# Performance work log

Hardware: AMD Instinct MI355X
Metric: run time of the kernel (lower is better)

Reference implementation:

```python
import jax, jax.numpy as jnp
import numpy as np
from jax import lax

EPS = 1e-12  # F.normalize eps


def conv3x3(x, w, b):
    # x [B,C,H,W], w [O,C,3,3], b [O]
    y = lax.conv_general_dilated(x, w, window_strides=(1, 1), padding=((1, 1), (1, 1)),
                                 dimension_numbers=("NCHW", "OIHW", "NCHW"))
    return y + b[None, :, None, None]


def bilinear_sample(img, py, px):
    # img [B,C,H,W]; py,px [B,H,W] fractional pixel coords; zero outside.
    B, C, H, W = img.shape
    y0 = jnp.floor(py)
    x0 = jnp.floor(px)
    img_flat = img.reshape(B, C, H * W)
    out = jnp.zeros_like(img)
    for dy in (0, 1):
        for dx in (0, 1):
            yi = y0 + dy
            xi = x0 + dx
            wgt = (1.0 - jnp.abs(py - yi)) * (1.0 - jnp.abs(px - xi))
            valid = (yi >= 0) & (yi < H) & (xi >= 0) & (xi < W)
            yc = jnp.clip(yi, 0, H - 1).astype(jnp.int32)
            xc = jnp.clip(xi, 0, W - 1).astype(jnp.int32)
            idx = (yc * W + xc).reshape(B, 1, H * W)
            v = jnp.take_along_axis(img_flat, idx, axis=2).reshape(B, C, H, W)
            out = out + v * (wgt * valid.astype(img.dtype))[:, None]
    return out


def deform_conv3x3(x, offset, weight):
    # torchvision deform_conv2d, k=3, stride=1, pad=1, no mask (modulator unused in source).
    # offset [B, 18, H, W]: per kernel tap k -> (dy=offset[:,2k], dx=offset[:,2k+1])
    B, Cin, H, W = x.shape
    iy = jnp.arange(H, dtype=x.dtype)[:, None]
    ix = jnp.arange(W, dtype=x.dtype)[None, :]
    out = jnp.zeros((B, weight.shape[0], H, W), dtype=x.dtype)
    for k in range(9):
        kh, kw = k // 3, k % 3
        py = iy - 1 + kh + offset[:, 2 * k]
        px = ix - 1 + kw + offset[:, 2 * k + 1]
        s = bilinear_sample(x, py, px)  # [B,Cin,H,W]
        out = out + jnp.einsum("bchw,oc->bohw", s, weight[:, :, kh, kw])
    return out


def l2norm_lastdim(t):
    n = jnp.sqrt(jnp.sum(t * t, axis=-1, keepdims=True))
    return t / jnp.maximum(n, EPS)


def setup_inputs() -> dict:
    key = jax.random.key(0)
    ks = jax.random.split(key, 8)
    B, C, H, W = 2, 192, 128, 128
    heads = 4
    s = 0.02
    return {
        "x": jax.random.normal(ks[0], (B, C, H, W), jnp.float32),
        "q": jax.random.normal(ks[1], (B, C, H, W), jnp.float32),
        "temperature": jnp.ones((1, heads, 1, 1), jnp.float32),
        "kv_w": jax.random.normal(ks[2], (2 * C, C), jnp.float32) * s,
        "offset_w": jax.random.normal(ks[3], (18, 2 * C, 3, 3), jnp.float32) * 0.001,
        "offset_b": jax.random.normal(ks[4], (18,), jnp.float32) * 0.1,
        "reg_w": jax.random.normal(ks[5], (2 * C, 2 * C, 3, 3), jnp.float32) * s,
        "proj_w": jax.random.normal(ks[6], (C, C), jnp.float32) * s,
    }


def reference(x, q, temperature, kv_w, offset_w, offset_b, reg_w, proj_w):
    B, C, H, W = x.shape
    heads = temperature.shape[1]
    n = H * W
    # kv 1x1 conv
    kv = jnp.einsum("bchw,oc->bohw", x, kv_w)  # [B,2C,H,W]
    # deformable conv KV path
    offset = conv3x3(kv, offset_w, offset_b)  # [B,18,H,W]
    kv = deform_conv3x3(kv, offset, reg_w)  # [B,2C,H,W]
    k, v = jnp.split(kv, 2, axis=1)
    qh = q.reshape(B, heads, C // heads, n)
    kh = k.reshape(B, heads, C // heads, n)
    vh = v.reshape(B, heads, C // heads, n)
    qh = l2norm_lastdim(qh)
    kh = l2norm_lastdim(kh)
    attn = jax.nn.softmax(jnp.einsum("bhdn,bhen->bhde", qh, kh) * temperature, axis=-1)
    out = jnp.einsum("bhde,bhen->bhdn", attn, vh).reshape(B, C, H, W)
    out = jnp.einsum("bchw,oc->bohw", out, proj_w)
    return (out, qh)
```

## Files before the change

kernel.cpp:

```cpp
#include <hip/hip_runtime.h>
#include <math.h>

#define B_ 2
#define C_ 192
#define C2_ 384
#define H_ 128
#define W_ 128
#define N_ (H_*W_)
#define HEADS_ 4
#define HD_ 48
#define EPS_ 1e-12f

typedef __bf16 bf16x8 __attribute__((ext_vector_type(8)));
typedef float  f32x4  __attribute__((ext_vector_type(4)));

__global__ __launch_bounds__(256) void k_pack(const float* __restrict__ regw, const float* __restrict__ kvw,
                                              const float* __restrict__ offw,
                                              ushort* __restrict__ regwP, ushort* __restrict__ kvwP,
                                              ushort* __restrict__ offwP) {
    const int NR = 9 * 12 * C2_ * 32;
    const int NK = 6 * C2_ * 32;
    const int NO = 12 * 9 * 32 * 32;
    int idx = blockIdx.x * 256 + threadIdx.x;
    union { __bf16 h; ushort u; } cv;
    if (idx < NR) {
        int t  = idx / (12 * C2_ * 32);
        int r  = idx - t * (12 * C2_ * 32);
        int ci = r / (C2_ * 32);
        int r2 = r - ci * (C2_ * 32);
        int oc = r2 >> 5;
        int kk = r2 & 31;
        cv.h = (__bf16)regw[(oc * C2_ + ci * 32 + kk) * 9 + t];
        regwP[idx] = cv.u;
    } else if (idx < NR + NK) {
        int r  = idx - NR;
        int ci = r / (C2_ * 32);
        int r2 = r - ci * (C2_ * 32);
        int oc = r2 >> 5;
        int kk = r2 & 31;
        cv.h = (__bf16)kvw[oc * C_ + ci * 32 + kk];
        kvwP[r] = cv.u;
    } else if (idx < NR + NK + NO) {
        int r  = idx - NR - NK;
        int ci = r / (9 * 32 * 32);
        int r2 = r - ci * (9 * 32 * 32);
        int t  = r2 / (32 * 32);
        int r3 = r2 - t * (32 * 32);
        int oc = r3 >> 5;
        int kk = r3 & 31;
        float v = (oc < 18) ? offw[(oc * C2_ + ci * 32 + kk) * 9 + t] : 0.f;
        cv.h = (__bf16)v;
        offwP[r] = cv.u;
    }
}

__global__ __launch_bounds__(256) void k_kv1x1_mfma(const float* __restrict__ x, const __bf16* __restrict__ kvwP,
                                                    __bf16* __restrict__ kvB) {
    __shared__ __bf16 As[64 * 40];
    __shared__ __bf16 Ws[C2_ * 40];
    const int bid = blockIdx.x;
    const int swz = (bid & 7) * 64 + (bid >> 3);
    const int b   = swz >> 8;
    const int p0  = (swz & 255) * 64;
    const int tid  = threadIdx.x;
    const int wv   = tid >> 6;
    const int lane = tid & 63;
    const int fr   = lane & 15;
    const int fg   = lane >> 4;
    const int apx  = tid & 63;
    const int akg  = tid >> 6;

    f32x4 acc[4][6];
    #pragma unroll
    for (int mg = 0; mg < 4; ++mg)
        #pragma unroll
        for (int ng = 0; ng < 6; ++ng) acc[mg][ng] = (f32x4){0.f, 0.f, 0.f, 0.f};

    for (int ci = 0; ci < 6; ++ci) {
        const int cc = ci * 32;
        const __bf16* wsrc = kvwP + (size_t)ci * C2_ * 32;
        #pragma unroll
        for (int i = 0; i < 6; ++i) {
            const int e = tid + i * 256;
            const int oc = e >> 2, sg = e & 3;
            *(bf16x8*)&Ws[oc * 40 + sg * 8] = *(const bf16x8*)(wsrc + oc * 32 + sg * 8);
        }
        {
            float v[8];
            #pragma unroll
            for (int j = 0; j < 8; ++j)
                v[j] = x[((size_t)b * C_ + cc + akg * 8 + j) * N_ + p0 + apx];
            bf16x8 pk = {(__bf16)v[0], (__bf16)v[1], (__bf16)v[2], (__bf16)v[3],
                         (__bf16)v[4], (__bf16)v[5], (__bf16)v[6], (__bf16)v[7]};
            *(bf16x8*)&As[apx * 40 + akg * 8] = pk;
        }
        __syncthreads();
        bf16x8 a[4];
        #pragma unroll
        for (int mg = 0; mg < 4; ++mg)
            a[mg] = *(const bf16x8*)&As[(mg * 16 + fr) * 40 + fg * 8];
        #pragma unroll
        for (int ng = 0; ng < 6; ++ng) {
            const bf16x8 bb = *(const bf16x8*)&Ws[(wv * 96 + ng * 16 + fr) * 40 + fg * 8];
            #pragma unroll
            for (int mg = 0; mg < 4; ++mg)
                acc[mg][ng] = __builtin_amdgcn_mfma_f32_16x16x32_bf16(a[mg], bb, acc[mg][ng], 0, 0, 0);
        }
        __syncthreads();
    }
    #pragma unroll
    for (int mg = 0; mg < 4; ++mg)
        #pragma unroll
        for (int j = 0; j < 4; ++j) {
            const int p = p0 + mg * 16 + fg * 4 + j;
            __bf16* dst = kvB + ((size_t)b * N_ + p) * C2_ + wv * 96 + fr;
            #pragma unroll
            for (int ng = 0; ng < 6; ++ng)
                dst[ng * 16] = (__bf16)acc[mg][ng][j];
        }
}

__global__ __launch_bounds__(256) void k_qnorm(const float* __restrict__ q, float* __restrict__ qn,
                                               __bf16* __restrict__ qnB) {
    const int row = blockIdx.x;
    const float* src = q + (size_t)row * N_;
    float* dst = qn + (size_t)row * N_;
    __bf16* dstB = qnB + (size_t)row * N_;
    float ss = 0.f;
    for (int i = threadIdx.x; i < N_ / 4; i += 256) {
        float4 v = ((const float4*)src)[i];
        ss += v.x * v.x + v.y * v.y + v.z * v.z + v.w * v.w;
    }
    __shared__ float red[256];
    red[threadIdx.x] = ss;
    __syncthreads();
    for (int s = 128; s > 0; s >>= 1) {
        if (threadIdx.x < s) red[threadIdx.x] += red[threadIdx.x + s];
        __syncthreads();
    }
    float rn = 1.f / fmaxf(sqrtf(red[0]), EPS_);
    for (int i = threadIdx.x; i < N_ / 8; i += 256) {
        float4 v0 = ((const float4*)src)[2 * i];
        float4 v1 = ((const float4*)src)[2 * i + 1];
        float f0 = v0.x * rn, f1 = v0.y * rn, f2 = v0.z * rn, f3 = v0.w * rn;
        float f4 = v1.x * rn, f5 = v1.y * rn, f6 = v1.z * rn, f7 = v1.w * rn;
        ((float4*)dst)[2 * i]     = make_float4(f0, f1, f2, f3);
        ((float4*)dst)[2 * i + 1] = make_float4(f4, f5, f6, f7);
        bf16x8 pk = {(__bf16)f0, (__bf16)f1, (__bf16)f2, (__bf16)f3,
                     (__bf16)f4, (__bf16)f5, (__bf16)f6, (__bf16)f7};
        *(bf16x8*)&dstB[i * 8] = pk;
    }
}

__global__ __launch_bounds__(256) void k_offconv_mfma(const __bf16* __restrict__ kvB, const __bf16* __restrict__ offwP,
                                                      const float* __restrict__ offb, float* __restrict__ offT) {
    __shared__ __bf16 Win[3 * 66 * 40];
    __shared__ __bf16 Wall[9 * 32 * 40];
    const int bid = blockIdx.x;
    const int swz = (bid & 7) * 64 + (bid >> 3);
    const int b   = swz >> 8;
    const int p0  = (swz & 255) * 64;
    const int y   = p0 >> 7;
    const int x0  = p0 & 127;
    const int tid  = threadIdx.x;
    const int wv   = tid >> 6;
    const int lane = tid & 63;
    const int fr   = lane & 15;
    const int fg   = lane >> 4;
    const __bf16* kb = kvB + (size_t)b * N_ * C2_;

    f32x4 acc[2];
    acc[0] = (f32x4){0.f, 0.f, 0.f, 0.f};
    acc[1] = (f32x4){0.f, 0.f, 0.f, 0.f};

    for (int ci = 0; ci < 12; ++ci) {
        const int cc = ci * 32;
        for (int e = tid; e < 3 * 66 * 4; e += 256) {
            const int r  = e / 264;
            const int rem = e - r * 264;
            const int cw = rem >> 2;
            const int sg = rem & 3;
            const int gy = y - 1 + r;
            const int gx = x0 - 1 + cw;
            bf16x8 v = {};
            if ((unsigned)gy < H_ && (unsigned)gx < W_)
                v = *(const bf16x8*)(kb + ((size_t)(gy * W_ + gx)) * C2_ + cc + sg * 8);
            *(bf16x8*)&Win[(r * 66 + cw) * 40 + sg * 8] = v;
        }
        const __bf16* wsrc = offwP + (size_t)ci * 9 * 32 * 32;
        for (int e = tid; e < 9 * 32 * 4; e += 256) {
            const int t  = e >> 7;
            const int r2 = e & 127;
            const int oc = r2 >> 2;
            const int sg = r2 & 3;
            *(bf16x8*)&Wall[(t * 32 + oc) * 40 + sg * 8] = *(const bf16x8*)(wsrc + (t * 32 + oc) * 32 + sg * 8);
        }
        __syncthreads();
        #pragma unroll
        for (int t = 0; t < 9; ++t) {
            const int dy = t / 3, dx = t % 3;
            const bf16x8 a = *(const bf16x8*)&Win[((dy * 66) + (wv * 16 + fr + dx)) * 40 + fg * 8];
            #pragma unroll
            for (int ng = 0; ng < 2; ++ng) {
                const bf16x8 bb = *(const bf16x8*)&Wall[(t * 32 + ng * 16 + fr) * 40 + fg * 8];
                acc[ng] = __builtin_amdgcn_mfma_f32_16x16x32_bf16(a, bb, acc[ng], 0, 0, 0);
            }
        }
        __syncthreads();
    }
    #pragma unroll
    for (int ng = 0; ng < 2; ++ng) {
        const int oc = ng * 16 + fr;
        if (oc < 18) {
            const float bias = offb[oc];
            #pragma unroll
            for (int j = 0; j < 4; ++j) {
                const int p = p0 + wv * 16 + fg * 4 + j;
                offT[((size_t)b * N_ + p) * 18 + oc] = acc[ng][j] + bias;
            }
        }
    }
}

#define SAMPLE_A(ITN, NB) do {                                                           \
    const int tt_ = (ITN) / 12, ci_ = (ITN) - tt_ * 12;                                  \
    const __bf16* cb_ = kb + ci_ * 32 + ssub;                                            \
    float s_[8] = {0.f,0.f,0.f,0.f,0.f,0.f,0.f,0.f};                                     \
    _Pragma("unroll")                                                                    \
    for (int j_ = 0; j_ < 4; ++j_) {                                                     \
        const float w_ = sh.m.wwt[tt_][spx][j_];                                         \
        const bf16x8 v_ = *(const bf16x8*)(cb_ + (size_t)sh.m.widx[tt_][spx][j_] * C2_); \
        _Pragma("unroll")                                                                \
        for (int e_ = 0; e_ < 8; ++e_) s_[e_] += w_ * (float)v_[e_];                     \
    }                                                                                    \
    bf16x8 pk_ = {(__bf16)s_[0],(__bf16)s_[1],(__bf16)s_[2],(__bf16)s_[3],               \
                  (__bf16)s_[4],(__bf16)s_[5],(__bf16)s_[6],(__bf16)s_[7]};              \
    *(bf16x8*)&sh.m.As[NB][spx * 40 + ssub] = pk_;                                       \
} while (0)

#define DEF_BODY(CUR, NXT) do {                                                          \
    const int itn_ = (it < 107) ? it + 1 : 107;                                          \
    {   const __bf16* wb_ = wbase + (size_t)itn_ * (C2_ * 32);                           \
        _Pragma("unroll")                                                                \
        for (int ng_ = 0; ng_ < 6; ++ng_)                                                \
            bfr[NXT][ng_] = *(const bf16x8*)(wb_ + ng_ * 512); }                         \
    bf16x8 a_[4];                                                                        \
    _Pragma("unroll")                                                                    \
    for (int mg_ = 0; mg_ < 4; ++mg_)                                                    \
        a_[mg_] = *(const bf16x8*)&sh.m.As[CUR][(mg_ * 16 + fr) * 40 + fg * 8];          \
    SAMPLE_A(itn_, NXT);                                                                 \
    _Pragma("unroll")                                                                    \
    for (int ng_ = 0; ng_ < 6; ++ng_)                                                    \
        _Pragma("unroll")                                                                \
        for (int mg_ = 0; mg_ < 4; ++mg_)                                                \
            acc[mg_][ng_] = __builtin_amdgcn_mfma_f32_16x16x32_bf16(a_[mg_], bfr[CUR][ng_], acc[mg_][ng_], 0, 0, 0); \
    __syncthreads();                                                                     \
    ++it;                                                                                \
} while (0)

__global__ __launch_bounds__(256, 2) void k_deform_mfma(const __bf16* __restrict__ kvB, const float* __restrict__ offT,
                                                        const __bf16* __restrict__ regwP,
                                                        __bf16* __restrict__ kT, __bf16* __restrict__ vP) {
    __shared__ union {
        struct {
            __bf16 As[2][64 * 40];
            float  wwt[9][64][4];
            int    widx[9][64][4];
        } m;
        __bf16 kTs[192 * 72];
    } sh;
    const int bid = blockIdx.x;
    const int swz = (bid & 7) * 64 + (bid >> 3);
    const int b   = swz >> 8;
    const int p0  = (swz & 255) * 64;
    const int tid  = threadIdx.x;
    const int wv   = tid >> 6;
    const int lane = tid & 63;
    const int fr   = lane & 15;
    const int fg   = lane >> 4;
    const int spx  = tid >> 2;
    const int ssub = (tid & 3) * 8;
    const __bf16* kb    = kvB + (size_t)b * N_ * C2_;
    const __bf16* wbase = regwP + ((size_t)(wv * 96 + fr)) * 32 + fg * 8;

    f32x4 acc[4][6];
    #pragma unroll
    for (int mg = 0; mg < 4; ++mg)
        #pragma unroll
        for (int ng = 0; ng < 6; ++ng) acc[mg][ng] = (f32x4){0.f, 0.f, 0.f, 0.f};

    for (int e = tid; e < 576; e += 256) {
        const int tt = e >> 6, pp = e & 63;
        const int p = p0 + pp;
        const int yy = p >> 7, xx = p & 127;
        const float dy = offT[((size_t)b * N_ + p) * 18 + 2 * tt];
        const float dx = offT[((size_t)b * N_ + p) * 18 + 2 * tt + 1];
        const float py = (float)(yy + tt / 3 - 1) + dy;
        const float px = (float)(xx + tt % 3 - 1) + dx;
        const float fy = floorf(py), fx = floorf(px);
        const int y0 = (int)fy, x0i = (int)fx;
        const float ay = py - fy, ax = px - fx;
        #pragma unroll
        for (int j = 0; j < 4; ++j) {
            const int yi = y0 + (j >> 1);
            const int xi = x0i + (j & 1);
            const float wj = ((j >> 1) ? ay : 1.f - ay) * ((j & 1) ? ax : 1.f - ax);
            const bool v = ((unsigned)yi < H_) && ((unsigned)xi < W_);
            sh.m.wwt[tt][pp][j]  = v ? wj : 0.f;
            sh.m.widx[tt][pp][j] = v ? (yi * W_ + xi) : 0;
        }
    }
    bf16x8 bfr[2][6];
    #pragma unroll
    for (int ng = 0; ng < 6; ++ng) bfr[0][ng] = *(const bf16x8*)(wbase + ng * 512);
    __syncthreads();
    SAMPLE_A(0, 0);
    __syncthreads();

    int it = 0;
    for (int i2 = 0; i2 < 54; ++i2) {
        DEF_BODY(0, 1);
        DEF_BODY(1, 0);
    }

    __syncthreads();
    if (wv < 2) {
        #pragma unroll
        for (int mg = 0; mg < 4; ++mg)
            #pragma unroll
            for (int ng = 0; ng < 6; ++ng) {
                const int oc = wv * 96 + ng * 16 + fr;
                #pragma unroll
                for (int j = 0; j < 4; ++j)
                    sh.kTs[oc * 72 + mg * 16 + fg * 4 + j] = (__bf16)acc[mg][ng][j];
            }
    } else {
        #pragma unroll
        for (int mg = 0; mg < 4; ++mg)
            #pragma unroll
            for (int j = 0; j < 4; ++j) {
                const int p = p0 + mg * 16 + fg * 4 + j;
                __bf16* dst = vP + ((size_t)b * N_ + p) * C_ + (wv - 2) * 96 + fr;
                #pragma unroll
                for (int ng = 0; ng < 6; ++ng)
                    dst[ng * 16] = (__bf16)acc[mg][ng][j];
            }
    }
    __syncthreads();
    for (int e = tid; e < 192 * 8; e += 256) {
        const int oc = e >> 3, sub = e & 7;
        *(bf16x8*)&kT[((size_t)b * C_ + oc) * N_ + p0 + sub * 8] = *(const bf16x8*)&sh.kTs[oc * 72 + sub * 8];
    }
}

__global__ __launch_bounds__(256) void k_knorm2(const __bf16* __restrict__ kT, float* __restrict__ knorm) {
    const int row = blockIdx.x;
    const __bf16* src = kT + (size_t)row * N_;
    float ss = 0.f;
    for (int i = threadIdx.x; i < N_ / 8; i += 256) {
        const bf16x8 v = ((const bf16x8*)src)[i];
        #pragma unroll
        for (int e = 0; e < 8; ++e) { float f = (float)v[e]; ss += f * f; }
    }
    __shared__ float red[256];
    red[threadIdx.x] = ss;
    __syncthreads();
    for (int s = 128; s > 0; s >>= 1) {
        if (threadIdx.x < s) red[threadIdx.x] += red[threadIdx.x + s];
        __syncthreads();
    }
    if (threadIdx.x == 0) knorm[row] = 1.f / fmaxf(sqrtf(red[0]), EPS_);
}

__global__ __launch_bounds__(256) void k_attn_mfma(const __bf16* __restrict__ qnB, const __bf16* __restrict__ kT,
                                                   float* __restrict__ part) {
    const int bh = blockIdx.y;
    const int b  = bh >> 2, h = bh & 3;
    const int wv = threadIdx.x >> 6, lane = threadIdx.x & 63;
    const int sl = blockIdx.x * 4 + wv;
    const int n0 = sl * 128;
    const int fr = lane & 15, fg = lane >> 4;
    const __bf16* qb = qnB + ((size_t)b * C_ + h * HD_) * N_ + n0 + fg * 8;
    const __bf16* kb = kT  + ((size_t)b * C_ + h * HD_) * N_ + n0 + fg * 8;
    f32x4 acc[3][3];
    #pragma unroll
    for (int i = 0; i < 3; ++i)
        #pragma unroll
        for (int j = 0; j < 3; ++j) acc[i][j] = (f32x4){0.f, 0.f, 0.f, 0.f};
    #pragma unroll
    for (int kc = 0; kc < 4; ++kc) {
        bf16x8 a[3], bb[3];
        #pragma unroll
        for (int mg = 0; mg < 3; ++mg) a[mg]  = *(const bf16x8*)(qb + (size_t)(mg * 16 + fr) * N_ + kc * 32);
        #pragma unroll
        for (int ng = 0; ng < 3; ++ng) bb[ng] = *(const bf16x8*)(kb + (size_t)(ng * 16 + fr) * N_ + kc * 32);
        #pragma unroll
        for (int mg = 0; mg < 3; ++mg)
            #pragma unroll
            for (int ng = 0; ng < 3; ++ng)
                acc[mg][ng] = __builtin_amdgcn_mfma_f32_16x16x32_bf16(a[mg], bb[ng], acc[mg][ng], 0, 0, 0);
    }
    float* pp = part + ((size_t)bh * 128 + sl) * (HD_ * HD_);
    #pragma unroll
    for (int mg = 0; mg < 3; ++mg)
        #pragma unroll
        for (int ng = 0; ng < 3; ++ng)
            #pragma unroll
            for (int j = 0; j < 4; ++j)
                pp[(mg * 16 + fg * 4 + j) * HD_ + ng * 16 + fr] = acc[mg][ng][j];
}

__global__ __launch_bounds__(256) void k_softmax(const float* __restrict__ part, const float* __restrict__ knorm,
                                                 const float* __restrict__ temp, float* __restrict__ attn) {
    const int row = blockIdx.x;
    const int b = row / (HEADS_ * HD_);
    const int r = row % (HEADS_ * HD_);
    const int h = r / HD_;
    const int d = r % HD_;
    const int bh = b * HEADS_ + h;
    const int wv = threadIdx.x >> 6;
    const int lane = threadIdx.x & 63;
    __shared__ float red[4][HD_];
    if (lane < HD_) {
        const float* pp = part + (size_t)bh * 128 * (HD_ * HD_) + d * HD_ + lane;
        float s = 0.f;
        for (int sl = wv; sl < 128; sl += 4)
            s += pp[(size_t)sl * (HD_ * HD_)];
        red[wv][lane] = s;
    }
    __syncthreads();
    if (wv == 0) {
        float v = -INFINITY;
        if (lane < HD_) {
            float t = red[0][lane] + red[1][lane] + red[2][lane] + red[3][lane];
            v = t * knorm[b * C_ + h * HD_ + lane] * temp[h];
        }
        float m = v;
        #pragma unroll
        for (int off = 32; off > 0; off >>= 1) m = fmaxf(m, __shfl_xor(m, off));
        float ex = (lane < HD_) ? expf(v - m) : 0.f;
        float sum = ex;
        #pragma unroll
        for (int off = 32; off > 0; off >>= 1) sum += __shfl_xor(sum, off);
        if (lane < HD_)
            attn[((size_t)bh * HD_ + d) * HD_ + lane] = ex / sum;
    }
}

__global__ __launch_bounds__(256) void k_m(const float* __restrict__ projw, const float* __restrict__ attn,
                                           __bf16* __restrict__ MmB) {
    const int gid = blockIdx.x * 256 + threadIdx.x;
    if (gid >= B_ * C_ * C_) return;
    const int b  = gid / (C_ * C_);
    const int r  = gid % (C_ * C_);
    const int oc = r / C_;
    const int he = r % C_;
    const int h = he / HD_;
    const int e = he % HD_;
    float s = 0.f;
    #pragma unroll 8
    for (int d = 0; d < HD_; ++d)
        s += projw[oc * C_ + h * HD_ + d] * attn[(((size_t)b * HEADS_ + h) * HD_ + d) * HD_ + e];
    MmB[gid] = (__bf16)s;
}

__global__ __launch_bounds__(256) void k_out_mfma(const __bf16* __restrict__ MmB, const __bf16* __restrict__ vP,
                                                  float* __restrict__ out) {
    const int bid = blockIdx.x;
    const int swz = (bid & 7) * 64 + (bid >> 3);
    const int b   = swz >> 8;
    const int p0  = (swz & 255) * 64;
    const int wv = threadIdx.x >> 6, lane = threadIdx.x & 63;
    const int fr = lane & 15, fg = lane >> 4;
    const __bf16* vb = vP + ((size_t)b * N_ + p0 + wv * 16 + fr) * C_ + fg * 8;
    const __bf16* mb = MmB + ((size_t)b * C_ + fr) * C_ + fg * 8;
    f32x4 acc[12];
    #pragma unroll
    for (int rr = 0; rr < 12; ++rr) acc[rr] = (f32x4){0.f, 0.f, 0.f, 0.f};
    #pragma unroll
    for (int kc = 0; kc < 6; ++kc) {
        const bf16x8 bb = *(const bf16x8*)(vb + kc * 32);
        #pragma unroll
        for (int rr = 0; rr < 12; ++rr) {
            const bf16x8 a = *(const bf16x8*)(mb + (size_t)(rr * 16) * C_ + kc * 32);
            acc[rr] = __builtin_amdgcn_mfma_f32_16x16x32_bf16(a, bb, acc[rr], 0, 0, 0);
        }
    }
    #pragma unroll
    for (int rr = 0; rr < 12; ++rr)
        #pragma unroll
        for (int j = 0; j < 4; ++j)
            out[((size_t)b * C_ + rr * 16 + fg * 4 + j) * N_ + p0 + wv * 16 + fr] = acc[rr][j];
}

extern "C" void kernel_launch(void* const* d_in, const int* in_sizes, int n_in,
                              void* d_out, int out_size, void* d_ws, size_t ws_size,
                              hipStream_t stream) {
    (void)in_sizes; (void)n_in; (void)out_size; (void)ws_size;
    const float* x     = (const float*)d_in[0];
    const float* q     = (const float*)d_in[1];
    const float* temp  = (const float*)d_in[2];
    const float* kvw   = (const float*)d_in[3];
    const float* offw  = (const float*)d_in[4];
    const float* offb  = (const float*)d_in[5];
    const float* regw  = (const float*)d_in[6];
    const float* projw = (const float*)d_in[7];

    float* out = (float*)d_out;
    float* qn  = out + (size_t)B_ * C_ * N_;
    __bf16* kvB = (__bf16*)out;

    ushort* kT    = (ushort*)d_ws;
    ushort* vP    = kT + (size_t)B_ * C_ * N_;
    float*  offT  = (float*)(vP + (size_t)B_ * C_ * N_);
    ushort* regwP = (ushort*)(offT + (size_t)B_ * N_ * 18);
    ushort* kvwP  = regwP + (size_t)9 * 12 * C2_ * 32;
    ushort* offwP = kvwP + (size_t)6 * C2_ * 32;
    ushort* qnB   = offwP + (size_t)12 * 9 * 32 * 32;
    float*  part  = (float*)(qnB + (size_t)B_ * C_ * N_);
    float*  attn  = part + (size_t)B_ * HEADS_ * 128 * HD_ * HD_;
    float*  knorm = attn + (size_t)B_ * HEADS_ * HD_ * HD_;
    ushort* MmB   = (ushort*)(knorm + (size_t)B_ * C_);

    const int packN = 9 * 12 * C2_ * 32 + 6 * C2_ * 32 + 12 * 9 * 32 * 32;
    k_pack<<<dim3((packN + 255) / 256), 256, 0, stream>>>(regw, kvw, offw, regwP, kvwP, offwP);
    k_kv1x1_mfma<<<dim3(N_ / 64 * B_), 256, 0, stream>>>(x, (const __bf16*)kvwP, kvB);
    k_offconv_mfma<<<dim3(N_ / 64 * B_), 256, 0, stream>>>(kvB, (const __bf16*)offwP, offb, offT);
    k_deform_mfma<<<dim3(N_ / 64 * B_), 256, 0, stream>>>(kvB, offT, (const __bf16*)regwP,
                                                          (__bf16*)kT, (__bf16*)vP);
    k_qnorm<<<dim3(B_ * C_), 256, 0, stream>>>(q, qn, (__bf16*)qnB);
    k_knorm2<<<dim3(B_ * C_), 256, 0, stream>>>((const __bf16*)kT, knorm);
    k_attn_mfma<<<dim3(32, B_ * HEADS_), 256, 0, stream>>>((const __bf16*)qnB, (const __bf16*)kT, part);
    k_softmax<<<dim3(B_ * HEADS_ * HD_), 256, 0, stream>>>(part, knorm, temp, attn);
    k_m<<<dim3((B_ * C_ * C_ + 255) / 256), 256, 0, stream>>>(projw, attn, (__bf16*)MmB);
    k_out_mfma<<<dim3(N_ / 64 * B_), 256, 0, stream>>>((const __bf16*)MmB, (const __bf16*)vP, out);
}
```

Measured before the change: 264.8 us.

## Prefetch deformable gather one iteration ahead and vectorize shared-memory loads

The bilinear gather for the deformable-conv A tile is split into an issue step and a pack step, so the global gathers for iteration i+2 are in flight while the MFMAs for iteration i run. Gather indices and weights are now read from shared memory as int4/float4 vectors. The k-transpose store to shared memory is packed into bf16x4 writes. Gather latency is meant to be hidden behind compute, at the cost of holding four more bf16x8 registers in each thread, which could hurt occupancy at launch bounds (256,2).

```diff
diff --git a/kernel.cpp b/kernel.cpp
--- a/kernel.cpp
+++ b/kernel.cpp
@@ -12,6 +12,7 @@
 #define EPS_ 1e-12f
 
 typedef __bf16 bf16x8 __attribute__((ext_vector_type(8)));
+typedef __bf16 bf16x4 __attribute__((ext_vector_type(4)));
 typedef float  f32x4  __attribute__((ext_vector_type(4)));
 
 __global__ __launch_bounds__(256) void k_pack(const float* __restrict__ regw, const float* __restrict__ kvw,
@@ -222,16 +223,26 @@
     }
 }
 
-#define SAMPLE_A(ITN, NB) do {                                                           \
+
+#define ISSUE_GATHER(ITN) do {                                                           \
     const int tt_ = (ITN) / 12, ci_ = (ITN) - tt_ * 12;                                  \
+    const int4 id4_ = *(const int4*)&sh.m.widx[tt_][spx][0];                             \
     const __bf16* cb_ = kb + ci_ * 32 + ssub;                                            \
+    graw[0] = *(const bf16x8*)(cb_ + (size_t)id4_.x * C2_);                              \
+    graw[1] = *(const bf16x8*)(cb_ + (size_t)id4_.y * C2_);                              \
+    graw[2] = *(const bf16x8*)(cb_ + (size_t)id4_.z * C2_);                              \
+    graw[3] = *(const bf16x8*)(cb_ + (size_t)id4_.w * C2_);                              \
+} while (0)
+
+#define PACK_A(ITN, NB) do {                                                             \
+    const int tt_ = (ITN) / 12;                                                          \
+    const float4 w4_ = *(const float4*)&sh.m.wwt[tt_][spx][0];                           \
+    const float wj_[4] = {w4_.x, w4_.y, w4_.z, w4_.w};                                   \
     float s_[8] = {0.f,0.f,0.f,0.f,0.f,0.f,0.f,0.f};                                     \
     _Pragma("unroll")                                                                    \
     for (int j_ = 0; j_ < 4; ++j_) {                                                     \
-        const float w_ = sh.m.wwt[tt_][spx][j_];                                         \
-        const bf16x8 v_ = *(const bf16x8*)(cb_ + (size_t)sh.m.widx[tt_][spx][j_] * C2_); \
         _Pragma("unroll")                                                                \
-        for (int e_ = 0; e_ < 8; ++e_) s_[e_] += w_ * (float)v_[e_];                     \
+        for (int e_ = 0; e_ < 8; ++e_) s_[e_] += wj_[j_] * (float)graw[j_][e_];          \
     }                                                                                    \
     bf16x8 pk_ = {(__bf16)s_[0],(__bf16)s_[1],(__bf16)s_[2],(__bf16)s_[3],               \
                   (__bf16)s_[4],(__bf16)s_[5],(__bf16)s_[6],(__bf16)s_[7]};              \
@@ -239,8 +250,9 @@
 } while (0)
 
 #define DEF_BODY(CUR, NXT) do {                                                          \
-    const int itn_ = (it < 107) ? it + 1 : 107;                                          \
-    {   const __bf16* wb_ = wbase + (size_t)itn_ * (C2_ * 32);                           \
+    const int ip1_ = (it < 107) ? it + 1 : 107;                                          \
+    const int ip2_ = (it < 106) ? it + 2 : 107;                                          \
+    {   const __bf16* wb_ = wbase + (size_t)ip1_ * (C2_ * 32);                           \
         _Pragma("unroll")                                                                \
         for (int ng_ = 0; ng_ < 6; ++ng_)                                                \
             bfr[NXT][ng_] = *(const bf16x8*)(wb_ + ng_ * 512); }                         \
@@ -248,7 +260,8 @@
     _Pragma("unroll")                                                                    \
     for (int mg_ = 0; mg_ < 4; ++mg_)                                                    \
         a_[mg_] = *(const bf16x8*)&sh.m.As[CUR][(mg_ * 16 + fr) * 40 + fg * 8];          \
-    SAMPLE_A(itn_, NXT);                                                                 \
+    PACK_A(ip1_, NXT);                                                                   \
+    ISSUE_GATHER(ip2_);                                                                  \
     _Pragma("unroll")                                                                    \
     for (int ng_ = 0; ng_ < 6; ++ng_)                                                    \
         _Pragma("unroll")                                                                \
@@ -310,11 +323,15 @@
             sh.m.widx[tt][pp][j] = v ? (yi * W_ + xi) : 0;
         }
     }
+    __syncthreads();
+
+    bf16x8 graw[4];
     bf16x8 bfr[2][6];
+    ISSUE_GATHER(0);
+    PACK_A(0, 0);
+    ISSUE_GATHER(1);
     #pragma unroll
     for (int ng = 0; ng < 6; ++ng) bfr[0][ng] = *(const bf16x8*)(wbase + ng * 512);
-    __syncthreads();
-    SAMPLE_A(0, 0);
     __syncthreads();
 
     int it = 0;
@@ -330,9 +347,9 @@
             #pragma unroll
             for (int ng = 0; ng < 6; ++ng) {
                 const int oc = wv * 96 + ng * 16 + fr;
-                #pragma unroll
-                for (int j = 0; j < 4; ++j)
-                    sh.kTs[oc * 72 + mg * 16 + fg * 4 + j] = (__bf16)acc[mg][ng][j];
+                const bf16x4 pk = {(__bf16)acc[mg][ng][0], (__bf16)acc[mg][ng][1],
+                                   (__bf16)acc[mg][ng][2], (__bf16)acc[mg][ng][3]};
+                *(bf16x4*)&sh.kTs[oc * 72 + mg * 16 + fg * 4] = pk;
             }
     } else {
         #pragma unroll
```

New measurement: 250.2 us. -5.5%, faster.

## Restructure deform conv so each wave samples its own pixels and fuse k-norm partials

Applied to the files above, without the earlier changes.

The deformable conv kernel is reorganized so that each wave owns 16 pixels and all 384 output channels. It samples its A fragment straight into registers, removing the shared-memory A double buffer and the per-iteration block barriers. The B weights are now loaded per wave for all 24 N-groups rather than split across waves, which raises global/L2 weight traffic and register pressure. The k-channel sum of squares is computed in the epilogue as per-block partials, so the full pass over kT in the norm kernel becomes a small reduction.

```diff
diff --git a/kernel.cpp b/kernel.cpp
--- a/kernel.cpp
+++ b/kernel.cpp
@@ -12,6 +12,7 @@
 #define EPS_ 1e-12f
 
 typedef __bf16 bf16x8 __attribute__((ext_vector_type(8)));
+typedef __bf16 bf16x4 __attribute__((ext_vector_type(4)));
 typedef float  f32x4  __attribute__((ext_vector_type(4)));
 
 __global__ __launch_bounds__(256) void k_pack(const float* __restrict__ regw, const float* __restrict__ kvw,
@@ -222,72 +223,34 @@
     }
 }
 
-#define SAMPLE_A(ITN, NB) do {                                                           \
-    const int tt_ = (ITN) / 12, ci_ = (ITN) - tt_ * 12;                                  \
-    const __bf16* cb_ = kb + ci_ * 32 + ssub;                                            \
-    float s_[8] = {0.f,0.f,0.f,0.f,0.f,0.f,0.f,0.f};                                     \
-    _Pragma("unroll")                                                                    \
-    for (int j_ = 0; j_ < 4; ++j_) {                                                     \
-        const float w_ = sh.m.wwt[tt_][spx][j_];                                         \
-        const bf16x8 v_ = *(const bf16x8*)(cb_ + (size_t)sh.m.widx[tt_][spx][j_] * C2_); \
-        _Pragma("unroll")                                                                \
-        for (int e_ = 0; e_ < 8; ++e_) s_[e_] += w_ * (float)v_[e_];                     \
-    }                                                                                    \
-    bf16x8 pk_ = {(__bf16)s_[0],(__bf16)s_[1],(__bf16)s_[2],(__bf16)s_[3],               \
-                  (__bf16)s_[4],(__bf16)s_[5],(__bf16)s_[6],(__bf16)s_[7]};              \
-    *(bf16x8*)&sh.m.As[NB][spx * 40 + ssub] = pk_;                                       \
-} while (0)
-
-#define DEF_BODY(CUR, NXT) do {                                                          \
-    const int itn_ = (it < 107) ? it + 1 : 107;                                          \
-    {   const __bf16* wb_ = wbase + (size_t)itn_ * (C2_ * 32);                           \
-        _Pragma("unroll")                                                                \
-        for (int ng_ = 0; ng_ < 6; ++ng_)                                                \
-            bfr[NXT][ng_] = *(const bf16x8*)(wb_ + ng_ * 512); }                         \
-    bf16x8 a_[4];                                                                        \
-    _Pragma("unroll")                                                                    \
-    for (int mg_ = 0; mg_ < 4; ++mg_)                                                    \
-        a_[mg_] = *(const bf16x8*)&sh.m.As[CUR][(mg_ * 16 + fr) * 40 + fg * 8];          \
-    SAMPLE_A(itn_, NXT);                                                                 \
-    _Pragma("unroll")                                                                    \
-    for (int ng_ = 0; ng_ < 6; ++ng_)                                                    \
-        _Pragma("unroll")                                                                \
-        for (int mg_ = 0; mg_ < 4; ++mg_)                                                \
-            acc[mg_][ng_] = __builtin_amdgcn_mfma_f32_16x16x32_bf16(a_[mg_], bfr[CUR][ng_], acc[mg_][ng_], 0, 0, 0); \
-    __syncthreads();                                                                     \
-    ++it;                                                                                \
-} while (0)
-
 __global__ __launch_bounds__(256, 2) void k_deform_mfma(const __bf16* __restrict__ kvB, const float* __restrict__ offT,
                                                         const __bf16* __restrict__ regwP,
-                                                        __bf16* __restrict__ kT, __bf16* __restrict__ vP) {
+                                                        __bf16* __restrict__ kT, __bf16* __restrict__ vP,
+                                                        float* __restrict__ knp) {
     __shared__ union {
         struct {
-            __bf16 As[2][64 * 40];
-            float  wwt[9][64][4];
-            int    widx[9][64][4];
+            float wwt[9][64][4];
+            int   widx[9][64][4];
         } m;
         __bf16 kTs[192 * 72];
     } sh;
     const int bid = blockIdx.x;
     const int swz = (bid & 7) * 64 + (bid >> 3);
-    const int b   = swz >> 8;
-    const int p0  = (swz & 255) * 64;
+    const int b    = swz >> 8;
+    const int pblk = swz & 255;
+    const int p0   = pblk * 64;
     const int tid  = threadIdx.x;
     const int wv   = tid >> 6;
     const int lane = tid & 63;
     const int fr   = lane & 15;
     const int fg   = lane >> 4;
-    const int spx  = tid >> 2;
-    const int ssub = (tid & 3) * 8;
-    const __bf16* kb    = kvB + (size_t)b * N_ * C2_;
-    const __bf16* wbase = regwP + ((size_t)(wv * 96 + fr)) * 32 + fg * 8;
-
-    f32x4 acc[4][6];
-    #pragma unroll
-    for (int mg = 0; mg < 4; ++mg)
-        #pragma unroll
-        for (int ng = 0; ng < 6; ++ng) acc[mg][ng] = (f32x4){0.f, 0.f, 0.f, 0.f};
+    const int pxl  = wv * 16 + fr;
+    const __bf16* kb  = kvB + (size_t)b * N_ * C2_ + fg * 8;
+    const __bf16* bb0 = regwP + fr * 32 + fg * 8;
+
+    f32x4 acc[24];
+    #pragma unroll
+    for (int ng = 0; ng < 24; ++ng) acc[ng] = (f32x4){0.f, 0.f, 0.f, 0.f};
 
     for (int e = tid; e < 576; e += 256) {
         const int tt = e >> 6, pp = e & 63;
@@ -310,41 +273,80 @@
             sh.m.widx[tt][pp][j] = v ? (yi * W_ + xi) : 0;
         }
     }
-    bf16x8 bfr[2][6];
-    #pragma unroll
-    for (int ng = 0; ng < 6; ++ng) bfr[0][ng] = *(const bf16x8*)(wbase + ng * 512);
     __syncthreads();
-    SAMPLE_A(0, 0);
+
+    const float4* wwp = (const float4*)&sh.m.wwt[0][pxl][0];
+    const int4*   wip = (const int4*)&sh.m.widx[0][pxl][0];
+
+    bf16x8 g[4];
+    {
+        const int4 id4 = wip[0];
+        g[0] = *(const bf16x8*)(kb + (size_t)id4.x * C2_);
+        g[1] = *(const bf16x8*)(kb + (size_t)id4.y * C2_);
+        g[2] = *(const bf16x8*)(kb + (size_t)id4.z * C2_);
+        g[3] = *(const bf16x8*)(kb + (size_t)id4.w * C2_);
+    }
+
+    int tt = 0, ci = 0;
+    for (int q = 0; q < 108; ++q) {
+        const float4 w4 = wwp[tt * 64];
+        float s[8] = {0.f, 0.f, 0.f, 0.f, 0.f, 0.f, 0.f, 0.f};
+        {
+            const float wj[4] = {w4.x, w4.y, w4.z, w4.w};
+            #pragma unroll
+            for (int j = 0; j < 4; ++j)
+                #pragma unroll
+                for (int e = 0; e < 8; ++e) s[e] += wj[j] * (float)g[j][e];
+        }
+        const bf16x8 aF = {(__bf16)s[0], (__bf16)s[1], (__bf16)s[2], (__bf16)s[3],
+                           (__bf16)s[4], (__bf16)s[5], (__bf16)s[6], (__bf16)s[7]};
+        {
+            int ttn = tt, cin = ci + 1;
+            if (cin == 12) { cin = 0; ++ttn; }
+            if (q == 107) { ttn = tt; cin = ci; }
+            const int4 id4 = wip[ttn * 64];
+            const __bf16* cb = kb + cin * 32;
+            g[0] = *(const bf16x8*)(cb + (size_t)id4.x * C2_);
+            g[1] = *(const bf16x8*)(cb + (size_t)id4.y * C2_);
+            g[2] = *(const bf16x8*)(cb + (size_t)id4.z * C2_);
+            g[3] = *(const bf16x8*)(cb + (size_t)id4.w * C2_);
+        }
+        const __bf16* bq = bb0 + (size_t)q * (C2_ * 32);
+        #pragma unroll
+        for (int g4 = 0; g4 < 4; ++g4) {
+            bf16x8 bbv[6];
+            #pragma unroll
+            for (int n6 = 0; n6 < 6; ++n6)
+                bbv[n6] = *(const bf16x8*)(bq + (g4 * 6 + n6) * 512);
+            #pragma unroll
+            for (int n6 = 0; n6 < 6; ++n6)
+                acc[g4 * 6 + n6] = __builtin_amdgcn_mfma_f32_16x16x32_bf16(aF, bbv[n6], acc[g4 * 6 + n6], 0, 0, 0);
+        }
+        ++ci;
+        if (ci == 12) { ci = 0; ++tt; }
+    }
+
     __syncthreads();
-
-    int it = 0;
-    for (int i2 = 0; i2 < 54; ++i2) {
-        DEF_BODY(0, 1);
-        DEF_BODY(1, 0);
-    }
-
-    __syncthreads();
-    if (wv < 2) {
-        #pragma unroll
-        for (int mg = 0; mg < 4; ++mg)
-            #pragma unroll
-            for (int ng = 0; ng < 6; ++ng) {
-                const int oc = wv * 96 + ng * 16 + fr;
-                #pragma unroll
-                for (int j = 0; j < 4; ++j)
-                    sh.kTs[oc * 72 + mg * 16 + fg * 4 + j] = (__bf16)acc[mg][ng][j];
-            }
-    } else {
-        #pragma unroll
-        for (int mg = 0; mg < 4; ++mg)
-            #pragma unroll
-            for (int j = 0; j < 4; ++j) {
-                const int p = p0 + mg * 16 + fg * 4 + j;
-                __bf16* dst = vP + ((size_t)b * N_ + p) * C_ + (wv - 2) * 96 + fr;
-                #pragma unroll
-                for (int ng = 0; ng < 6; ++ng)
-                    dst[ng * 16] = (__bf16)acc[mg][ng][j];
-            }
+    #pragma unroll
+    for (int ng = 0; ng < 12; ++ng) {
+        const int oc = ng * 16 + fr;
+        const bf16x4 pk = {(__bf16)acc[ng][0], (__bf16)acc[ng][1],
+                           (__bf16)acc[ng][2], (__bf16)acc[ng][3]};
+        *(bf16x4*)&sh.kTs[oc * 72 + wv * 16 + fg * 4] = pk;
+        float ss = acc[ng][0] * acc[ng][0] + acc[ng][1] * acc[ng][1]
+                 + acc[ng][2] * acc[ng][2] + acc[ng][3] * acc[ng][3];
+        ss += __shfl_xor(ss, 16);
+        ss += __shfl_xor(ss, 32);
+        if (fg == 0) knp[((size_t)b * C_ + oc) * 1024 + pblk * 4 + wv] = ss;
+    }
+    #pragma unroll
+    for (int ng = 12; ng < 24; ++ng) {
+        const int voc = (ng - 12) * 16 + fr;
+        #pragma unroll
+        for (int j = 0; j < 4; ++j) {
+            const int p = p0 + wv * 16 + fg * 4 + j;
+            vP[((size_t)b * N_ + p) * C_ + voc] = (__bf16)acc[ng][j];
+        }
     }
     __syncthreads();
     for (int e = tid; e < 192 * 8; e += 256) {
@@ -353,20 +355,16 @@
     }
 }
 
-__global__ __launch_bounds__(256) void k_knorm2(const __bf16* __restrict__ kT, float* __restrict__ knorm) {
+__global__ __launch_bounds__(256) void k_knred(const float* __restrict__ knp, float* __restrict__ knorm) {
     const int row = blockIdx.x;
-    const __bf16* src = kT + (size_t)row * N_;
-    float ss = 0.f;
-    for (int i = threadIdx.x; i < N_ / 8; i += 256) {
-        const bf16x8 v = ((const bf16x8*)src)[i];
-        #pragma unroll
-        for (int e = 0; e < 8; ++e) { float f = (float)v[e]; ss += f * f; }
-    }
+    const float* src = knp + (size_t)row * 1024;
+    float s = 0.f;
+    for (int i = threadIdx.x; i < 1024; i += 256) s += src[i];
     __shared__ float red[256];
-    red[threadIdx.x] = ss;
+    red[threadIdx.x] = s;
     __syncthreads();
-    for (int s = 128; s > 0; s >>= 1) {
-        if (threadIdx.x < s) red[threadIdx.x] += red[threadIdx.x + s];
+    for (int st = 128; st > 0; st >>= 1) {
+        if (threadIdx.x < st) red[threadIdx.x] += red[threadIdx.x + st];
         __syncthreads();
     }
     if (threadIdx.x == 0) knorm[row] = 1.f / fmaxf(sqrtf(red[0]), EPS_);
@@ -521,15 +519,16 @@
     float*  attn  = part + (size_t)B_ * HEADS_ * 128 * HD_ * HD_;
     float*  knorm = attn + (size_t)B_ * HEADS_ * HD_ * HD_;
     ushort* MmB   = (ushort*)(knorm + (size_t)B_ * C_);
+    float*  knp   = (float*)(MmB + (size_t)B_ * C_ * C_);
 
     const int packN = 9 * 12 * C2_ * 32 + 6 * C2_ * 32 + 12 * 9 * 32 * 32;
     k_pack<<<dim3((packN + 255) / 256), 256, 0, stream>>>(regw, kvw, offw, regwP, kvwP, offwP);
     k_kv1x1_mfma<<<dim3(N_ / 64 * B_), 256, 0, stream>>>(x, (const __bf16*)kvwP, kvB);
     k_offconv_mfma<<<dim3(N_ / 64 * B_), 256, 0, stream>>>(kvB, (const __bf16*)offwP, offb, offT);
     k_deform_mfma<<<dim3(N_ / 64 * B_), 256, 0, stream>>>(kvB, offT, (const __bf16*)regwP,
-                                                          (__bf16*)kT, (__bf16*)vP);
+                                                          (__bf16*)kT, (__bf16*)vP, knp);
     k_qnorm<<<dim3(B_ * C_), 256, 0, stream>>>(q, qn, (__bf16*)qnB);
-    k_knorm2<<<dim3(B_ * C_), 256, 0, stream>>>((const __bf16*)kT, knorm);
+    k_knred<<<dim3(B_ * C_), 256, 0, stream>>>(knp, knorm);
     k_attn_mfma<<<dim3(32, B_ * HEADS_), 256, 0, stream>>>((const __bf16*)qnB, (const __bf16*)kT, part);
     k_softmax<<<dim3(B_ * HEADS_ * HD_), 256, 0, stream>>>(part, knorm, temp, attn);
     k_m<<<dim3((B_ * C_ * C_ + 255) / 256), 256, 0, stream>>>(projw, attn, (__bf16*)MmB);
```

After: 516.2 us. +94.9%, slower.
